# Optimization experiments

Measured on AMD Instinct MI355X. Metric: run time of the kernel, lower is better.

## Reference

```python
import jax, jax.numpy as jnp
import numpy as np

NB, NLOC, NALL, NNEI = 1, 4096, 6144, 64
N_EDGE, N_ANGLE, A_SEL = 262144, 409600, 10
N_DIM, E_DIM, A_DIM, AXIS = 128, 64, 32, 4
SEL_REDUCE = 10.0


def _lin_params(key, din, dout):
    k1, k2 = jax.random.split(key)
    W = jax.random.normal(k1, (din, dout), jnp.float32) / np.float32(np.sqrt(din))
    b = jax.random.normal(k2, (dout,), jnp.float32) * 0.01
    return W, b


def setup_inputs():
    key = jax.random.key(0)
    ks = jax.random.split(key, 20)
    inp = {}
    inp["node_ebd_ext"] = jax.random.normal(ks[0], (NB, NALL, N_DIM), jnp.float32)
    inp["edge_ebd"] = jax.random.normal(ks[1], (N_EDGE, E_DIM), jnp.float32)
    inp["h2"] = jax.random.normal(ks[2], (N_EDGE, 3), jnp.float32)
    inp["angle_ebd"] = jax.random.normal(ks[3], (N_ANGLE, A_DIM), jnp.float32)
    inp["nlist"] = jax.random.randint(ks[4], (NB, NLOC, NNEI), 0, NALL)
    inp["nlist_mask"] = jnp.ones((NB, NLOC, NNEI), jnp.bool_)
    inp["sw"] = jax.random.uniform(ks[5], (N_EDGE,), jnp.float32)
    inp["a_nlist"] = jax.random.randint(ks[6], (NB, NLOC, A_SEL), 0, NALL)
    inp["a_nlist_mask"] = jnp.ones((NB, NLOC, A_SEL), jnp.bool_)
    inp["a_sw"] = jax.random.uniform(ks[7], (N_ANGLE,), jnp.float32)
    n2e = jax.random.randint(ks[8], (N_EDGE,), 0, NB * NLOC)
    n_ext2e = jax.random.randint(ks[9], (N_EDGE,), 0, NB * NALL)
    inp["edge_index"] = jnp.stack([n2e, n_ext2e])
    n2a = jax.random.randint(ks[10], (N_ANGLE,), 0, NB * NLOC)
    eij2a = jax.random.randint(ks[11], (N_ANGLE,), 0, N_EDGE)
    eik2a = jax.random.randint(ks[12], (N_ANGLE,), 0, N_EDGE)
    inp["angle_index"] = jnp.stack([n2a, eij2a, eik2a])
    sym_dim = (N_DIM + E_DIM) * AXIS          # 768
    edge_info_dim = 2 * N_DIM + E_DIM         # 320
    angle_dim = A_DIM + N_DIM + 2 * E_DIM     # 288
    inp["W_node_self"], inp["b_node_self"] = _lin_params(ks[13], N_DIM, N_DIM)
    inp["W_node_sym"], inp["b_node_sym"] = _lin_params(ks[14], sym_dim, N_DIM)
    inp["W_node_edge"], inp["b_node_edge"] = _lin_params(ks[15], edge_info_dim, N_DIM)
    inp["W_edge_self"], inp["b_edge_self"] = _lin_params(ks[16], edge_info_dim, E_DIM)
    inp["W_edge_angle1"], inp["b_edge_angle1"] = _lin_params(ks[17], angle_dim, E_DIM)
    inp["W_edge_angle2"], inp["b_edge_angle2"] = _lin_params(ks[18], E_DIM, E_DIM)
    inp["W_angle_self"], inp["b_angle_self"] = _lin_params(ks[19], angle_dim, A_DIM)
    inp["n_res0"] = jnp.full((N_DIM,), 0.1, jnp.float32)
    inp["n_res1"] = jnp.full((N_DIM,), 0.1, jnp.float32)
    inp["n_res2"] = jnp.full((N_DIM,), 0.1, jnp.float32)
    inp["e_res0"] = jnp.full((E_DIM,), 0.1, jnp.float32)
    inp["e_res1"] = jnp.full((E_DIM,), 0.1, jnp.float32)
    inp["a_res0"] = jnp.full((A_DIM,), 0.1, jnp.float32)
    return inp


def reference(node_ebd_ext, edge_ebd, h2, angle_ebd, nlist, nlist_mask, sw,
              a_nlist, a_nlist_mask, a_sw, edge_index, angle_index,
              W_node_self, b_node_self, W_node_sym, b_node_sym,
              W_node_edge, b_node_edge, W_edge_self, b_edge_self,
              W_edge_angle1, b_edge_angle1, W_edge_angle2, b_edge_angle2,
              W_angle_self, b_angle_self,
              n_res0, n_res1, n_res2, e_res0, e_res1, a_res0):
    act = jax.nn.silu
    nb, nloc, nnei = nlist.shape
    n_dim = node_ebd_ext.shape[-1]
    n_edge = h2.shape[0]
    dyn_e_sel = nnei / SEL_REDUCE
    dyn_a_sel = a_nlist.shape[-1] / SEL_REDUCE
    node_ebd = node_ebd_ext[:, :nloc]
    n2e, n_ext2e = edge_index[0], edge_index[1]
    n2a, eij2a, eik2a = angle_index[0], angle_index[1], angle_index[2]
    nei_node_ebd = node_ebd_ext.reshape(-1, n_dim)[n_ext2e]  # [n_edge, n_dim]
    node_self = act(node_ebd @ W_node_self + b_node_self)

    def sym_op(flat_ebd):
        # symmetrization: outer(h2, sw*ebd) scattered to owners, then grrg
        d = flat_ebd.shape[-1]
        w = flat_ebd * sw[:, None]
        h2g2 = jax.ops.segment_sum(
            (h2[:, :, None] * w[:, None, :]).reshape(n_edge, 3 * d),
            n2e, num_segments=nb * nloc)
        h2g2 = h2g2.reshape(nb, nloc, 3, d) * (dyn_e_sel ** -0.5)
        m = h2g2[..., :AXIS]  # [nb, nloc, 3, axis]
        g = jnp.einsum('blxa,blxd->blad', m, h2g2) / 3.0
        return g.reshape(nb, nloc, AXIS * d)

    sym_edge = sym_op(edge_ebd)
    sym_node = sym_op(nei_node_ebd)
    node_sym = act(jnp.concatenate([sym_edge, sym_node], -1) @ W_node_sym + b_node_sym)
    node_i = node_ebd.reshape(-1, n_dim)[n2e]
    edge_info = jnp.concatenate([node_i, nei_node_ebd, edge_ebd], -1)  # [n_edge, 320]
    node_edge_update = act(edge_info @ W_node_edge + b_node_edge) * sw[:, None]
    node_edge_msg = jax.ops.segment_sum(node_edge_update, n2e, num_segments=nb * nloc).reshape(nb, nloc, -1) / dyn_e_sel
    n_updated = node_ebd + n_res0 * node_self + n_res1 * node_sym + n_res2 * node_edge_msg
    edge_self = act(edge_info @ W_edge_self + b_edge_self)
    node_for_angle = node_ebd.reshape(-1, n_dim)[n2a]
    edge_ik = edge_ebd[eik2a]
    edge_ij = edge_ebd[eij2a]
    angle_info = jnp.concatenate([angle_ebd, node_for_angle, edge_ik, edge_ij], -1)  # [n_angle, 288]
    edge_angle = act(angle_info @ W_edge_angle1 + b_edge_angle1)
    reduced = jax.ops.segment_sum(edge_angle * a_sw[:, None], eij2a, num_segments=n_edge) / (dyn_a_sel ** 0.5)
    edge_angle_msg = act(reduced @ W_edge_angle2 + b_edge_angle2)
    e_updated = edge_ebd + e_res0 * edge_self + e_res1 * edge_angle_msg
    angle_self = act(angle_info @ W_angle_self + b_angle_self)
    a_updated = angle_ebd + a_res0 * angle_self
    return (n_updated, e_updated, a_updated)
```

## Files before the change

kernel.cpp:

```cpp
#include <hip/hip_runtime.h>
#include <hip/hip_bf16.h>

#define NLOC_   4096
#define NALL_   6144
#define NEDGE_  262144
#define NANGLE_ 409600

typedef __bf16 bf16x8 __attribute__((ext_vector_type(8)));
typedef float  f32x4  __attribute__((ext_vector_type(4)));
typedef unsigned short u16;

__device__ __forceinline__ float silu_(float x){ return x / (1.0f + __expf(-x)); }

__device__ __forceinline__ u16 f2bu(float f){
    union { float f; unsigned u; } v; v.f = f;
    unsigned r = v.u + 0x7fffu + ((v.u >> 16) & 1u);
    return (u16)(r >> 16);
}
__device__ __forceinline__ float bu2f(u16 b){
    union { unsigned u; float f; } v; v.u = ((unsigned)b) << 16; return v.f;
}
__device__ __forceinline__ void st_bf16x4(u16* dst, float4 v){
    unsigned lo = (unsigned)f2bu(v.x) | ((unsigned)f2bu(v.y) << 16);
    unsigned hi = (unsigned)f2bu(v.z) | ((unsigned)f2bu(v.w) << 16);
    *reinterpret_cast<uint2*>(dst) = make_uint2(lo, hi);
}

__global__ void k_prep(const float* __restrict__ Wne, const float* __restrict__ Wes,
                       const float* __restrict__ W1,  const float* __restrict__ WA,
                       const float* __restrict__ W2,
                       u16* __restrict__ WTe, u16* __restrict__ WTa, u16* __restrict__ WT2)
{
    int b = blockIdx.x, t = threadIdx.x;
    if (b < 192) {
        if (t < 320) WTe[b*320 + t] = f2bu(b < 128 ? Wne[t*128 + b] : Wes[t*64 + (b-128)]);
    } else if (b < 288) {
        int n = b - 192;
        if (t < 288) WTa[n*288 + t] = f2bu(n < 64 ? W1[t*64 + n] : WA[t*32 + (n-64)]);
    } else {
        int n = b - 288;
        if (t < 64)  WT2[n*64 + t] = f2bu(W2[t*64 + n]);
    }
}

__global__ void k_cvt(const float* __restrict__ src, u16* __restrict__ dst, int n4)
{
    int i = blockIdx.x * 256 + threadIdx.x;
    int stride = gridDim.x * 256;
    for (; i < n4; i += stride) {
        float4 v = ((const float4*)src)[i];
        st_bf16x4(&dst[(size_t)i*4], v);
    }
}

__global__ __launch_bounds__(256) void k_nconst(
    const u16* __restrict__ NB, const u16* __restrict__ WTe,
    float* __restrict__ nconst)
{
    __shared__ __align__(16) u16 sN[64][136];
    const int tid = threadIdx.x;
    const int e0 = blockIdx.x * 64;
    #pragma unroll
    for (int f = tid; f < 1024; f += 256) {
        int r = f >> 4, c = f & 15;
        *(uint4*)&sN[r][8*c] = ((const uint4*)&NB[(size_t)(e0 + r)*128])[c];
    }
    __syncthreads();

    const int w = tid >> 6, l = tid & 63;
    const int lr = l & 15, hq = l >> 4, lk = hq * 8;

    f32x4 acc[4][3] = {};
    #pragma unroll
    for (int kk = 0; kk < 4; ++kk) {
        bf16x8 a[4], b[3];
        #pragma unroll
        for (int m = 0; m < 4; ++m)
            a[m] = *(const bf16x8*)&sN[16*m + lr][kk*32 + lk];
        #pragma unroll
        for (int nf = 0; nf < 3; ++nf)
            b[nf] = *(const bf16x8*)&WTe[(size_t)(48*w + 16*nf + lr)*320 + kk*32 + lk];
        #pragma unroll
        for (int m = 0; m < 4; ++m)
            #pragma unroll
            for (int nf = 0; nf < 3; ++nf)
                acc[m][nf] = __builtin_amdgcn_mfma_f32_16x16x32_bf16(a[m], b[nf], acc[m][nf], 0, 0, 0);
    }
    #pragma unroll
    for (int nf = 0; nf < 3; ++nf) {
        int c = 48*w + 16*nf + lr;
        #pragma unroll
        for (int m = 0; m < 4; ++m)
            #pragma unroll
            for (int j = 0; j < 4; ++j) {
                int r = 16*m + 4*hq + j;
                nconst[(size_t)(e0 + r)*192 + c] = acc[m][nf][j];
            }
    }
}

__global__ void k_count(const int* __restrict__ key, int* __restrict__ cnt)
{
    int e = blockIdx.x * 256 + threadIdx.x;
    atomicAdd(&cnt[key[e]], 1);
}

__global__ void k_scan(const int* __restrict__ cnt, int* __restrict__ off,
                       int* __restrict__ cursor)
{
    __shared__ int wa[1024];
    int t = threadIdx.x;
    int a0 = cnt[4*t], a1 = cnt[4*t+1], a2 = cnt[4*t+2], a3 = cnt[4*t+3];
    int s1 = a0 + a1, s2 = s1 + a2, s3 = s2 + a3;
    wa[t] = s3;
    __syncthreads();
    for (int d = 1; d < 1024; d <<= 1) {
        int x = wa[t];
        int y = (t >= d) ? wa[t-d] : 0;
        __syncthreads();
        wa[t] = x + y;
        __syncthreads();
    }
    int excl = (t == 0) ? 0 : wa[t-1];
    off[4*t]   = excl;        cursor[4*t]   = excl;
    off[4*t+1] = excl + a0;   cursor[4*t+1] = excl + a0;
    off[4*t+2] = excl + s1;   cursor[4*t+2] = excl + s1;
    off[4*t+3] = excl + s2;   cursor[4*t+3] = excl + s2;
    if (t == 1023) off[4096] = excl + s3;
}

__global__ void k_fill(const int* __restrict__ key, int* __restrict__ cursor,
                       int* __restrict__ csr)
{
    int e = blockIdx.x * 256 + threadIdx.x;
    int pos = atomicAdd(&cursor[key[e]], 1);
    csr[pos] = e;
}

__global__ void k_fill_rank(const int* __restrict__ key, int* __restrict__ cursor,
                            int* __restrict__ rank)
{
    int e = blockIdx.x * 256 + threadIdx.x;
    int pos = atomicAdd(&cursor[key[e]], 1);
    rank[e] = pos;
}

__global__ void k_scan2a(const int* __restrict__ cnt2, int* __restrict__ bsum)
{
    __shared__ int wa[256];
    int b = blockIdx.x, t = threadIdx.x;
    int4 v = ((const int4*)cnt2)[b*256 + t];
    wa[t] = v.x + v.y + v.z + v.w;
    __syncthreads();
    for (int d = 128; d > 0; d >>= 1) {
        if (t < d) wa[t] += wa[t+d];
        __syncthreads();
    }
    if (t == 0) bsum[b] = wa[0];
}

__global__ void k_scan2b(const int* __restrict__ bsum, int* __restrict__ boff)
{
    __shared__ int wa[256];
    int t = threadIdx.x;
    wa[t] = bsum[t];
    __syncthreads();
    for (int d = 1; d < 256; d <<= 1) {
        int x = wa[t];
        int y = (t >= d) ? wa[t-d] : 0;
        __syncthreads();
        wa[t] = x + y;
        __syncthreads();
    }
    boff[t] = (t == 0) ? 0 : wa[t-1];
}

__global__ void k_scan2c(const int* __restrict__ cnt2, const int* __restrict__ boff,
                         int* __restrict__ off2, int* __restrict__ cursor2)
{
    __shared__ int wa[256];
    int b = blockIdx.x, t = threadIdx.x;
    int4 v = ((const int4*)cnt2)[b*256 + t];
    int s1 = v.x, s2 = s1 + v.y, s3 = s2 + v.z, s4 = s3 + v.w;
    wa[t] = s4;
    __syncthreads();
    for (int d = 1; d < 256; d <<= 1) {
        int x = wa[t];
        int y = (t >= d) ? wa[t-d] : 0;
        __syncthreads();
        wa[t] = x + y;
        __syncthreads();
    }
    int base = boff[b] + ((t == 0) ? 0 : wa[t-1]);
    int i = (b*256 + t)*4;
    off2[i]   = base;      cursor2[i]   = base;
    off2[i+1] = base + s1; cursor2[i+1] = base + s1;
    off2[i+2] = base + s2; cursor2[i+2] = base + s2;
    off2[i+3] = base + s3; cursor2[i+3] = base + s3;
    if (b == 255 && t == 255) off2[NEDGE_] = NANGLE_;
}

__global__ __launch_bounds__(256, 4) void k_edge_flat(
    const u16* __restrict__ NB, const u16* __restrict__ EB,
    const float* __restrict__ h2, const float* __restrict__ sw,
    const int* __restrict__ n2e, const int* __restrict__ n_ext2e,
    const int* __restrict__ csr,
    const u16* __restrict__ WTe, const float* __restrict__ nconst,
    const float* __restrict__ bne, const float* __restrict__ bes,
    const float* __restrict__ e_res0,
    float* __restrict__ msg,
    float* __restrict__ h2g2_e, float* __restrict__ h2g2_n,
    float* __restrict__ e_out)
{
    __shared__ __align__(16) u16 sA[64][200];
    __shared__ float sH[4][576];
    __shared__ int   s_eid[64];
    __shared__ int   s_node[64];
    __shared__ int   s_g[64];
    __shared__ float s_sw[64];
    __shared__ float s_h2[64][3];
    __shared__ int   s_segstart[65];
    __shared__ int   s_nseg;

    const int tid = threadIdx.x;
    const int w  = tid >> 6, l = tid & 63;
    const int lr = l & 15, hq = l >> 4, lk = hq * 8;
    const int base = blockIdx.x * 64;

    if (tid < 64) {
        int e = csr[base + tid];
        s_eid[tid]  = e;
        s_node[tid] = n2e[e];
        s_g[tid]    = n_ext2e[e];
        s_sw[tid]   = sw[e];
        s_h2[tid][0] = h2[e*3];
        s_h2[tid][1] = h2[e*3+1];
        s_h2[tid][2] = h2[e*3+2];
    }
    __syncthreads();

    if (tid < 64) {
        bool flag = (tid == 0) || (s_node[tid] != s_node[tid-1]);
        unsigned long long mask = __ballot(flag);
        if (flag) {
            int sid = __popcll(mask & ((1ull << tid) - 1ull));
            s_segstart[sid] = tid;
        }
        if (tid == 0) {
            int ns = __popcll(mask);
            s_nseg = ns;
            s_segstart[ns] = 64;
        }
    }

    #pragma unroll
    for (int f = tid; f < 1024; f += 256) {
        int r = f >> 4, c = f & 15;
        *(uint4*)&sA[r][8*c] = ((const uint4*)&NB[(size_t)s_g[r]*128])[c];
    }
    #pragma unroll
    for (int f = tid; f < 512; f += 256) {
        int r = f >> 3, c = f & 7;
        *(uint4*)&sA[r][128 + 8*c] = ((const uint4*)&EB[(size_t)s_eid[r]*64])[c];
    }
    __syncthreads();

    float bias[3], rres[3];
    int   cful[3];
    #pragma unroll
    for (int nf = 0; nf < 3; ++nf) {
        int c = 48*w + 16*nf + lr;
        cful[nf] = c;
        bias[nf] = (c < 128) ? bne[c] : bes[c-128];
        rres[nf] = (c < 128) ? 0.f    : e_res0[c-128];
    }

    f32x4 acc[4][3] = {};
    #pragma unroll
    for (int kk = 0; kk < 6; ++kk) {
        bf16x8 a[4], b[3];
        #pragma unroll
        for (int m = 0; m < 4; ++m)
            a[m] = *(const bf16x8*)&sA[16*m + lr][kk*32 + lk];
        #pragma unroll
        for (int nf = 0; nf < 3; ++nf)
            b[nf] = *(const bf16x8*)&WTe[(size_t)cful[nf]*320 + 128 + kk*32 + lk];
        #pragma unroll
        for (int m = 0; m < 4; ++m)
            #pragma unroll
            for (int nf = 0; nf < 3; ++nf)
                acc[m][nf] = __builtin_amdgcn_mfma_f32_16x16x32_bf16(a[m], b[nf], acc[m][nf], 0, 0, 0);
    }

    #pragma unroll
    for (int nf = 0; nf < 3; ++nf) {
        int c = cful[nf];
        if (c < 128) {
            #pragma unroll
            for (int m = 0; m < 4; ++m)
                #pragma unroll
                for (int j = 0; j < 4; ++j) {
                    int r = 16*m + 4*hq + j;
                    float ncv = nconst[(size_t)s_node[r]*192 + c];
                    acc[m][nf][j] = silu_(acc[m][nf][j] + ncv + bias[nf]) * s_sw[r];
                }
        } else {
            int c2 = c - 128;
            #pragma unroll
            for (int m = 0; m < 4; ++m)
                #pragma unroll
                for (int j = 0; j < 4; ++j) {
                    int r = 16*m + 4*hq + j;
                    float ncv = nconst[(size_t)s_node[r]*192 + c];
                    e_out[(size_t)s_eid[r]*64 + c2] =
                        bu2f(sA[r][128 + c2]) + rres[nf] * silu_(acc[m][nf][j] + ncv + bias[nf]);
                }
        }
    }

    const int nseg = s_nseg;
    for (int s = 0; s < nseg; ++s) {
        int rs = s_segstart[s], re = s_segstart[s+1];
        int nd = s_node[rs];
        #pragma unroll
        for (int nf = 0; nf < 3; ++nf) {
            if (cful[nf] >= 128) continue;
            float v = 0.f;
            #pragma unroll
            for (int m = 0; m < 4; ++m)
                #pragma unroll
                for (int j = 0; j < 4; ++j) {
                    int r = 16*m + 4*hq + j;
                    v += (r >= rs && r < re) ? acc[m][nf][j] : 0.f;
                }
            v += __shfl_xor(v, 16);
            v += __shfl_xor(v, 32);
            if (hq == 0) atomicAdd(&msg[(size_t)nd*128 + cful[nf]], v);
        }
    }

    for (int s = 0; s < nseg; ++s) {
        int rs = s_segstart[s], re = s_segstart[s+1];
        int nd = s_node[rs];
        int lo = max(16*w, rs), hi = min(16*w + 16, re);
        float hacc[9] = {0.f,0.f,0.f,0.f,0.f,0.f,0.f,0.f,0.f};
        for (int r = lo; r < hi; ++r) {
            float swv = s_sw[r];
            float s0 = s_h2[r][0] * swv;
            float s1 = s_h2[r][1] * swv;
            float s2 = s_h2[r][2] * swv;
            float eb = bu2f(sA[r][128 + l]);
            float n0 = bu2f(sA[r][l]);
            float n1 = bu2f(sA[r][64 + l]);
            hacc[0] = fmaf(s0, eb, hacc[0]);
            hacc[1] = fmaf(s1, eb, hacc[1]);
            hacc[2] = fmaf(s2, eb, hacc[2]);
            hacc[3] = fmaf(s0, n0, hacc[3]);
            hacc[4] = fmaf(s0, n1, hacc[4]);
            hacc[5] = fmaf(s1, n0, hacc[5]);
            hacc[6] = fmaf(s1, n1, hacc[6]);
            hacc[7] = fmaf(s2, n0, hacc[7]);
            hacc[8] = fmaf(s2, n1, hacc[8]);
        }
        #pragma unroll
        for (int q = 0; q < 3; ++q) sH[w][q*64 + l] = hacc[q];
        #pragma unroll
        for (int q = 0; q < 6; ++q) sH[w][192 + q*64 + l] = hacc[3+q];
        __syncthreads();
        for (int i = tid; i < 576; i += 256) {
            float v = sH[0][i] + sH[1][i] + sH[2][i] + sH[3][i];
            if (i < 192) atomicAdd(&h2g2_e[(size_t)nd*192 + i], v);
            else         atomicAdd(&h2g2_n[(size_t)nd*384 + (i - 192)], v);
        }
        __syncthreads();
    }
}

__global__ __launch_bounds__(256) void k_angle_mfma(
    const u16* __restrict__ NB, const u16* __restrict__ EB,
    const u16* __restrict__ AB, const float* __restrict__ a_sw,
    const int* __restrict__ n2a, const int* __restrict__ eij2a,
    const int* __restrict__ eik2a, const int* __restrict__ rank2,
    const u16* __restrict__ WTa,
    const float* __restrict__ b1, const float* __restrict__ bA,
    const float* __restrict__ a_res0,
    u16* __restrict__ ea, float* __restrict__ a_out)
{
    __shared__ __align__(16) u16 sA[64][296];
    __shared__ int s_na[64], s_ij[64], s_ik[64], s_rk[64];
    const int tid = threadIdx.x;
    const int a0 = blockIdx.x * 64;

    if (tid < 64) {
        s_na[tid] = n2a[a0 + tid];
        s_ij[tid] = eij2a[a0 + tid];
        s_ik[tid] = eik2a[a0 + tid];
        s_rk[tid] = rank2[a0 + tid];
    }
    __syncthreads();

    #pragma unroll
    for (int f = tid; f < 256; f += 256) {
        int a = f >> 2, c = f & 3;
        *(uint4*)&sA[a][8*c] = ((const uint4*)&AB[(size_t)(a0 + a)*32])[c];
    }
    #pragma unroll
    for (int f = tid; f < 1024; f += 256) {
        int a = f >> 4, c = f & 15;
        *(uint4*)&sA[a][32 + 8*c] = ((const uint4*)&NB[(size_t)s_na[a]*128])[c];
    }
    #pragma unroll
    for (int f = tid; f < 512; f += 256) {
        int a = f >> 3, c = f & 7;
        *(uint4*)&sA[a][160 + 8*c] = ((const uint4*)&EB[(size_t)s_ik[a]*64])[c];
    }
    #pragma unroll
    for (int f = tid; f < 512; f += 256) {
        int a = f >> 3, c = f & 7;
        *(uint4*)&sA[a][224 + 8*c] = ((const uint4*)&EB[(size_t)s_ij[a]*64])[c];
    }
    __syncthreads();

    const int w = tid >> 6, l = tid & 63;
    const int lr = l & 15, lk = (l >> 4) * 8;

    f32x4 acc[6] = {};
    #pragma unroll
    for (int kk = 0; kk < 9; ++kk) {
        bf16x8 a = *(const bf16x8*)&sA[16*w + lr][kk*32 + lk];
        #pragma unroll
        for (int n = 0; n < 6; ++n) {
            bf16x8 b = *(const bf16x8*)&WTa[(size_t)(16*n + lr)*288 + kk*32 + lk];
            acc[n] = __builtin_amdgcn_mfma_f32_16x16x32_bf16(a, b, acc[n], 0, 0, 0);
        }
    }

    #pragma unroll
    for (int n = 0; n < 6; ++n) {
        int c = 16*n + lr;
        if (n < 4) {
            float bb = b1[c];
            #pragma unroll
            for (int j = 0; j < 4; ++j) {
                int r = 16*w + ((l >> 4) << 2) + j;
                float eav = silu_(acc[n][j] + bb) * a_sw[a0 + r];
                ea[(size_t)s_rk[r]*64 + c] = f2bu(eav);
            }
        } else {
            int c2 = c - 64;
            float bb = bA[c2], rr = a_res0[c2];
            #pragma unroll
            for (int j = 0; j < 4; ++j) {
                int r = 16*w + ((l >> 4) << 2) + j;
                size_t idx = (size_t)(a0 + r)*32 + c2;
                a_out[idx] = bu2f(sA[r][c2]) + rr * silu_(acc[n][j] + bb);
            }
        }
    }
}

__global__ __launch_bounds__(256) void k_edgefin_mfma(
    const u16* __restrict__ ea,
    const int* __restrict__ off2,
    const u16* __restrict__ WT2,
    const float* __restrict__ b2_, const float* __restrict__ e_res1,
    float* __restrict__ e_out)
{
    __shared__ __align__(16) u16 sR[64][72];
    const int tid = threadIdx.x;
    const int e0 = blockIdx.x * 64;
    const int w = tid >> 6, l = tid & 63;

    #pragma unroll
    for (int r16 = 0; r16 < 16; ++r16) {
        int r = w*16 + r16;
        int e = e0 + r;
        float s = 0.f;
        int jb = off2[e], je = off2[e+1];
        for (int j = jb; j < je; ++j)
            s += bu2f(ea[(size_t)j*64 + l]);
        sR[r][l] = f2bu(s);
    }
    __syncthreads();

    const int lr = l & 15, lk = (l >> 4) * 8;

    f32x4 acc[4] = {};
    #pragma unroll
    for (int kk = 0; kk < 2; ++kk) {
        bf16x8 b = *(const bf16x8*)&WT2[(size_t)(16*w + lr)*64 + kk*32 + lk];
        #pragma unroll
        for (int m = 0; m < 4; ++m) {
            bf16x8 a = *(const bf16x8*)&sR[16*m + lr][kk*32 + lk];
            acc[m] = __builtin_amdgcn_mfma_f32_16x16x32_bf16(a, b, acc[m], 0, 0, 0);
        }
    }
    int c = 16*w + lr;
    float bb = b2_[c], rr = e_res1[c];
    #pragma unroll
    for (int m = 0; m < 4; ++m)
        #pragma unroll
        for (int j = 0; j < 4; ++j) {
            size_t idx = (size_t)(e0 + 16*m + ((l >> 4) << 2) + j)*64 + c;
            e_out[idx] += rr * silu_(acc[m][j] + bb);
        }
}

__global__ void k_node_final(const float* __restrict__ node_ext,
                             const float* __restrict__ h2g2_e,
                             const float* __restrict__ h2g2_n,
                             const float* __restrict__ msg,
                             const float* __restrict__ Wns,  const float* __restrict__ bns,
                             const float* __restrict__ Wsym, const float* __restrict__ bsym,
                             const float* __restrict__ nr0, const float* __restrict__ nr1,
                             const float* __restrict__ nr2,
                             float* __restrict__ n_out)
{
    __shared__ float x[128];
    __shared__ float he[192];
    __shared__ float hn[384];
    __shared__ float symc[768];

    int n = blockIdx.x;
    int c = threadIdx.x;

    x[c] = node_ext[(size_t)n*128 + c];
    for (int i = c; i < 192; i += 128) he[i] = h2g2_e[(size_t)n*192 + i];
    for (int i = c; i < 384; i += 128) hn[i] = h2g2_n[(size_t)n*384 + i];
    __syncthreads();

    const float SCALE = 1.0f / (6.4f * 3.0f);
    for (int i = c; i < 768; i += 128) {
        float s;
        if (i < 256) {
            int a = i >> 6, j = i & 63;
            s = he[a]*he[j] + he[64+a]*he[64+j] + he[128+a]*he[128+j];
        } else {
            int i2 = i - 256;
            int a = i2 >> 7, j = i2 & 127;
            s = hn[a]*hn[j] + hn[128+a]*hn[128+j] + hn[256+a]*hn[256+j];
        }
        symc[i] = s * SCALE;
    }
    __syncthreads();

    float accs = 0.f;
    #pragma unroll 8
    for (int k = 0; k < 128; ++k) accs = fmaf(x[k], Wns[k*128 + c], accs);
    float self_ = silu_(accs + bns[c]);

    float accy = 0.f;
    #pragma unroll 8
    for (int k = 0; k < 768; ++k) accy = fmaf(symc[k], Wsym[k*128 + c], accy);
    float sym_ = silu_(accy + bsym[c]);

    float m = msg[(size_t)n*128 + c] * (1.0f / 6.4f);
    n_out[(size_t)n*128 + c] = x[c] + nr0[c]*self_ + nr1[c]*sym_ + nr2[c]*m;
}

extern "C" void kernel_launch(void* const* d_in, const int* in_sizes, int n_in,
                              void* d_out, int out_size, void* d_ws, size_t ws_size,
                              hipStream_t stream)
{
    const float* node_ext  = (const float*)d_in[0];
    const float* edge_ebd  = (const float*)d_in[1];
    const float* h2        = (const float*)d_in[2];
    const float* angle_ebd = (const float*)d_in[3];
    const float* sw        = (const float*)d_in[6];
    const float* a_sw      = (const float*)d_in[9];
    const int*  edge_index  = (const int*)d_in[10];
    const int*  angle_index = (const int*)d_in[11];
    const int* n2e     = edge_index;
    const int* n_ext2e = edge_index + NEDGE_;
    const int* n2a     = angle_index;
    const int* eij2a   = angle_index + NANGLE_;
    const int* eik2a   = angle_index + 2*NANGLE_;

    const float* Wns  = (const float*)d_in[12];
    const float* bns  = (const float*)d_in[13];
    const float* Wsym = (const float*)d_in[14];
    const float* bsym = (const float*)d_in[15];
    const float* Wne  = (const float*)d_in[16];
    const float* bne  = (const float*)d_in[17];
    const float* Wes  = (const float*)d_in[18];
    const float* bes  = (const float*)d_in[19];
    const float* W1   = (const float*)d_in[20];
    const float* b1   = (const float*)d_in[21];
    const float* W2   = (const float*)d_in[22];
    const float* b2_  = (const float*)d_in[23];
    const float* WA   = (const float*)d_in[24];
    const float* bA   = (const float*)d_in[25];
    const float* nr0  = (const float*)d_in[26];
    const float* nr1  = (const float*)d_in[27];
    const float* nr2  = (const float*)d_in[28];
    const float* er0  = (const float*)d_in[29];
    const float* er1  = (const float*)d_in[30];
    const float* ar0  = (const float*)d_in[31];

    char* wsp = (char*)d_ws;
    u16*   ea      = (u16*)wsp;    wsp += (size_t)NANGLE_ * 64 * 2;
    u16*   EB      = (u16*)wsp;    wsp += (size_t)NEDGE_ * 64 * 2;
    u16*   NB      = (u16*)wsp;    wsp += (size_t)NALL_ * 128 * 2;
    u16*   AB      = (u16*)wsp;    wsp += (size_t)NANGLE_ * 32 * 2;
    int*   cnt     = (int*)wsp;    wsp += 4096 * 4;
    int*   cnt2    = (int*)wsp;    wsp += (size_t)NEDGE_ * 4;
    float* msg     = (float*)wsp;  wsp += (size_t)NLOC_ * 128 * 4;
    float* h2g2_e  = (float*)wsp;  wsp += (size_t)NLOC_ * 192 * 4;
    float* h2g2_n  = (float*)wsp;  wsp += (size_t)NLOC_ * 384 * 4;
    size_t zero_bytes = 4096*4 + (size_t)NEDGE_*4 + (size_t)NLOC_*128*4
                      + (size_t)NLOC_*192*4 + (size_t)NLOC_*384*4;
    int*   off     = (int*)wsp;    wsp += 4104 * 4;
    int*   cursor  = (int*)wsp;    wsp += 4096 * 4;
    int*   csr     = (int*)wsp;    wsp += (size_t)NEDGE_ * 4;
    int*   off2    = (int*)wsp;    wsp += ((size_t)NEDGE_ + 16) * 4;
    int*   cursor2 = (int*)wsp;    wsp += (size_t)NEDGE_ * 4;
    int*   bsum    = (int*)wsp;    wsp += 256 * 4;
    int*   boff    = (int*)wsp;    wsp += 256 * 4;
    int*   rank2   = (int*)wsp;    wsp += (size_t)NANGLE_ * 4;
    float* nconst  = (float*)wsp;  wsp += (size_t)NLOC_ * 192 * 4;
    u16*   WTe     = (u16*)wsp;    wsp += 192 * 320 * 2;
    u16*   WTa     = (u16*)wsp;    wsp += 96 * 288 * 2;
    u16*   WT2     = (u16*)wsp;    wsp += 64 * 64 * 2;

    hipMemsetAsync(cnt, 0, zero_bytes, stream);

    float* n_out = (float*)d_out;
    float* e_out = n_out + (size_t)NLOC_ * 128;
    float* a_out = e_out + (size_t)NEDGE_ * 64;

    k_prep   <<<352, 320, 0, stream>>>(Wne, Wes, W1, WA, W2, WTe, WTa, WT2);
    k_cvt    <<<768, 256, 0, stream>>>(node_ext, NB, NALL_*128/4);
    k_cvt    <<<4096, 256, 0, stream>>>(edge_ebd, EB, NEDGE_*64/4);
    k_cvt    <<<4096, 256, 0, stream>>>(angle_ebd, AB, NANGLE_*32/4);
    k_count  <<<NEDGE_/256, 256, 0, stream>>>(n2e, cnt);
    k_scan   <<<1, 1024, 0, stream>>>(cnt, off, cursor);
    k_fill   <<<NEDGE_/256, 256, 0, stream>>>(n2e, cursor, csr);
    k_count  <<<NANGLE_/256, 256, 0, stream>>>(eij2a, cnt2);
    k_scan2a <<<256, 256, 0, stream>>>(cnt2, bsum);
    k_scan2b <<<1, 256, 0, stream>>>(bsum, boff);
    k_scan2c <<<256, 256, 0, stream>>>(cnt2, boff, off2, cursor2);
    k_fill_rank <<<NANGLE_/256, 256, 0, stream>>>(eij2a, cursor2, rank2);

    k_nconst <<<NLOC_/64, 256, 0, stream>>>(NB, WTe, nconst);
    k_edge_flat <<<NEDGE_/64, 256, 0, stream>>>(NB, EB, h2, sw, n2e, n_ext2e, csr,
                                                WTe, nconst, bne, bes, er0,
                                                msg, h2g2_e, h2g2_n, e_out);
    k_angle_mfma <<<NANGLE_/64, 256, 0, stream>>>(NB, EB, AB, a_sw,
                                                  n2a, eij2a, eik2a, rank2,
                                                  WTa, b1, bA, ar0, ea, a_out);
    k_edgefin_mfma <<<NEDGE_/64, 256, 0, stream>>>(ea, off2, WT2, b2_, er1, e_out);
    k_node_final <<<NLOC_, 128, 0, stream>>>(node_ext, h2g2_e, h2g2_n, msg,
                                             Wns, bns, Wsym, bsym,
                                             nr0, nr1, nr2, n_out);
}
```

Before: 497.5 us.

## Move node-final GEMMs to MFMA and restructure edge/angle output writes

Replaces the scalar per-node k_node_final with a k_symc kernel that writes the symmetric features as bf16, followed by a 32-row MFMA kernel for the sym and self linear layers. The edge self-update is now written to a bf16 buffer in CSR order. It is combined in k_edgefin with a coalesced read of the edge embedding through a new rank array, so e_out is written once rather than read-modify-written. The angle kernel drops to 32-row tiles and stages its scattered ea output in LDS so it can be written as 16-byte vectors. These changes add an extra kernel launch, an intermediate buffer and more bf16 rounding of intermediates.

```diff
diff --git a/kernel.cpp b/kernel.cpp
--- a/kernel.cpp
+++ b/kernel.cpp
@@ -28,8 +28,10 @@
 
 __global__ void k_prep(const float* __restrict__ Wne, const float* __restrict__ Wes,
                        const float* __restrict__ W1,  const float* __restrict__ WA,
-                       const float* __restrict__ W2,
-                       u16* __restrict__ WTe, u16* __restrict__ WTa, u16* __restrict__ WT2)
+                       const float* __restrict__ W2,  const float* __restrict__ Wsym,
+                       const float* __restrict__ Wns,
+                       u16* __restrict__ WTe, u16* __restrict__ WTa, u16* __restrict__ WT2,
+                       u16* __restrict__ WsymT, u16* __restrict__ WnsT)
 {
     int b = blockIdx.x, t = threadIdx.x;
     if (b < 192) {
@@ -37,9 +39,15 @@
     } else if (b < 288) {
         int n = b - 192;
         if (t < 288) WTa[n*288 + t] = f2bu(n < 64 ? W1[t*64 + n] : WA[t*32 + (n-64)]);
-    } else {
+    } else if (b < 352) {
         int n = b - 288;
         if (t < 64)  WT2[n*64 + t] = f2bu(W2[t*64 + n]);
+    } else if (b < 480) {
+        int n = b - 352;
+        if (t < 768) WsymT[n*768 + t] = f2bu(Wsym[t*128 + n]);
+    } else {
+        int n = b - 480;
+        if (t < 128) WnsT[n*128 + t] = f2bu(Wns[t*128 + n]);
     }
 }
 
@@ -129,12 +137,13 @@
     if (t == 1023) off[4096] = excl + s3;
 }
 
-__global__ void k_fill(const int* __restrict__ key, int* __restrict__ cursor,
-                       int* __restrict__ csr)
+__global__ void k_fill_both(const int* __restrict__ key, int* __restrict__ cursor,
+                            int* __restrict__ csr, int* __restrict__ rank)
 {
     int e = blockIdx.x * 256 + threadIdx.x;
     int pos = atomicAdd(&cursor[key[e]], 1);
     csr[pos] = e;
+    rank[e] = pos;
 }
 
 __global__ void k_fill_rank(const int* __restrict__ key, int* __restrict__ cursor,
@@ -207,10 +216,9 @@
     const int* __restrict__ csr,
     const u16* __restrict__ WTe, const float* __restrict__ nconst,
     const float* __restrict__ bne, const float* __restrict__ bes,
-    const float* __restrict__ e_res0,
     float* __restrict__ msg,
     float* __restrict__ h2g2_e, float* __restrict__ h2g2_n,
-    float* __restrict__ e_out)
+    u16* __restrict__ eselfB)
 {
     __shared__ __align__(16) u16 sA[64][200];
     __shared__ float sH[4][576];
@@ -265,14 +273,13 @@
     }
     __syncthreads();
 
-    float bias[3], rres[3];
+    float bias[3];
     int   cful[3];
     #pragma unroll
     for (int nf = 0; nf < 3; ++nf) {
         int c = 48*w + 16*nf + lr;
         cful[nf] = c;
         bias[nf] = (c < 128) ? bne[c] : bes[c-128];
-        rres[nf] = (c < 128) ? 0.f    : e_res0[c-128];
     }
 
     f32x4 acc[4][3] = {};
@@ -312,8 +319,8 @@
                 for (int j = 0; j < 4; ++j) {
                     int r = 16*m + 4*hq + j;
                     float ncv = nconst[(size_t)s_node[r]*192 + c];
-                    e_out[(size_t)s_eid[r]*64 + c2] =
-                        bu2f(sA[r][128 + c2]) + rres[nf] * silu_(acc[m][nf][j] + ncv + bias[nf]);
+                    eselfB[(size_t)(base + r)*64 + c2] =
+                        f2bu(silu_(acc[m][nf][j] + ncv + bias[nf]));
                 }
         }
     }
@@ -386,90 +393,115 @@
     const float* __restrict__ a_res0,
     u16* __restrict__ ea, float* __restrict__ a_out)
 {
-    __shared__ __align__(16) u16 sA[64][296];
-    __shared__ int s_na[64], s_ij[64], s_ik[64], s_rk[64];
+    __shared__ __align__(16) u16 sA[32][296];
+    __shared__ __align__(16) u16 sEA[32][64];
+    __shared__ int s_na[32], s_ij[32], s_ik[32], s_rk[32];
+    __shared__ float s_asw[32];
     const int tid = threadIdx.x;
-    const int a0 = blockIdx.x * 64;
-
-    if (tid < 64) {
+    const int a0 = blockIdx.x * 32;
+
+    if (tid < 32) {
         s_na[tid] = n2a[a0 + tid];
         s_ij[tid] = eij2a[a0 + tid];
         s_ik[tid] = eik2a[a0 + tid];
         s_rk[tid] = rank2[a0 + tid];
-    }
-    __syncthreads();
-
-    #pragma unroll
-    for (int f = tid; f < 256; f += 256) {
-        int a = f >> 2, c = f & 3;
-        *(uint4*)&sA[a][8*c] = ((const uint4*)&AB[(size_t)(a0 + a)*32])[c];
-    }
-    #pragma unroll
-    for (int f = tid; f < 1024; f += 256) {
-        int a = f >> 4, c = f & 15;
-        *(uint4*)&sA[a][32 + 8*c] = ((const uint4*)&NB[(size_t)s_na[a]*128])[c];
+        s_asw[tid] = a_sw[a0 + tid];
+    }
+    __syncthreads();
+
+    if (tid < 128) {
+        int r = tid >> 2, c = tid & 3;
+        *(uint4*)&sA[r][8*c] = ((const uint4*)&AB[(size_t)(a0 + r)*32])[c];
     }
     #pragma unroll
     for (int f = tid; f < 512; f += 256) {
-        int a = f >> 3, c = f & 7;
-        *(uint4*)&sA[a][160 + 8*c] = ((const uint4*)&EB[(size_t)s_ik[a]*64])[c];
-    }
-    #pragma unroll
-    for (int f = tid; f < 512; f += 256) {
-        int a = f >> 3, c = f & 7;
-        *(uint4*)&sA[a][224 + 8*c] = ((const uint4*)&EB[(size_t)s_ij[a]*64])[c];
+        int r = f >> 4, c = f & 15;
+        *(uint4*)&sA[r][32 + 8*c] = ((const uint4*)&NB[(size_t)s_na[r]*128])[c];
+    }
+    if (tid < 256) {
+        int r = tid >> 3, c = tid & 7;
+        *(uint4*)&sA[r][160 + 8*c] = ((const uint4*)&EB[(size_t)s_ik[r]*64])[c];
+    }
+    {
+        int f = tid;
+        if (f < 256) {
+            int r = f >> 3, c = f & 7;
+            *(uint4*)&sA[r][224 + 8*c] = ((const uint4*)&EB[(size_t)s_ij[r]*64])[c];
+        }
     }
     __syncthreads();
 
     const int w = tid >> 6, l = tid & 63;
-    const int lr = l & 15, lk = (l >> 4) * 8;
-
-    f32x4 acc[6] = {};
+    const int lr = l & 15, hq = l >> 4, lk = hq * 8;
+    const int mrow  = (w & 1) * 16;
+    const int nbase = (w >> 1) * 48;
+
+    f32x4 acc[3] = {};
     #pragma unroll
     for (int kk = 0; kk < 9; ++kk) {
-        bf16x8 a = *(const bf16x8*)&sA[16*w + lr][kk*32 + lk];
-        #pragma unroll
-        for (int n = 0; n < 6; ++n) {
-            bf16x8 b = *(const bf16x8*)&WTa[(size_t)(16*n + lr)*288 + kk*32 + lk];
-            acc[n] = __builtin_amdgcn_mfma_f32_16x16x32_bf16(a, b, acc[n], 0, 0, 0);
-        }
-    }
-
-    #pragma unroll
-    for (int n = 0; n < 6; ++n) {
-        int c = 16*n + lr;
-        if (n < 4) {
+        bf16x8 a = *(const bf16x8*)&sA[mrow + lr][kk*32 + lk];
+        #pragma unroll
+        for (int nf = 0; nf < 3; ++nf) {
+            bf16x8 b = *(const bf16x8*)&WTa[(size_t)(nbase + 16*nf + lr)*288 + kk*32 + lk];
+            acc[nf] = __builtin_amdgcn_mfma_f32_16x16x32_bf16(a, b, acc[nf], 0, 0, 0);
+        }
+    }
+
+    #pragma unroll
+    for (int nf = 0; nf < 3; ++nf) {
+        int c = nbase + 16*nf + lr;
+        if (c < 64) {
             float bb = b1[c];
             #pragma unroll
             for (int j = 0; j < 4; ++j) {
-                int r = 16*w + ((l >> 4) << 2) + j;
-                float eav = silu_(acc[n][j] + bb) * a_sw[a0 + r];
-                ea[(size_t)s_rk[r]*64 + c] = f2bu(eav);
+                int r = mrow + 4*hq + j;
+                sEA[r][c] = f2bu(silu_(acc[nf][j] + bb) * s_asw[r]);
             }
         } else {
             int c2 = c - 64;
             float bb = bA[c2], rr = a_res0[c2];
             #pragma unroll
             for (int j = 0; j < 4; ++j) {
-                int r = 16*w + ((l >> 4) << 2) + j;
+                int r = mrow + 4*hq + j;
                 size_t idx = (size_t)(a0 + r)*32 + c2;
-                a_out[idx] = bu2f(sA[r][c2]) + rr * silu_(acc[n][j] + bb);
+                a_out[idx] = bu2f(sA[r][c2]) + rr * silu_(acc[nf][j] + bb);
             }
         }
     }
+    __syncthreads();
+
+    if (tid < 256) {
+        int r = tid >> 3, c = tid & 7;
+        *(uint4*)&ea[(size_t)s_rk[r]*64 + 8*c] = *(const uint4*)&sEA[r][8*c];
+    }
 }
 
 __global__ __launch_bounds__(256) void k_edgefin_mfma(
-    const u16* __restrict__ ea,
-    const int* __restrict__ off2,
+    const u16* __restrict__ EB, const u16* __restrict__ eselfB,
+    const int* __restrict__ rank_e,
+    const u16* __restrict__ ea, const int* __restrict__ off2,
     const u16* __restrict__ WT2,
-    const float* __restrict__ b2_, const float* __restrict__ e_res1,
+    const float* __restrict__ b2_, const float* __restrict__ er0,
+    const float* __restrict__ er1,
     float* __restrict__ e_out)
 {
     __shared__ __align__(16) u16 sR[64][72];
+    __shared__ __align__(16) u16 sE[64][72];
+    __shared__ __align__(16) u16 sB[64][72];
+    __shared__ int s_rk[64];
     const int tid = threadIdx.x;
     const int e0 = blockIdx.x * 64;
     const int w = tid >> 6, l = tid & 63;
+
+    if (tid < 64) s_rk[tid] = rank_e[e0 + tid];
+    __syncthreads();
+
+    #pragma unroll
+    for (int f = tid; f < 512; f += 256) {
+        int r = f >> 3, c = f & 7;
+        *(uint4*)&sB[r][8*c] = ((const uint4*)&EB[(size_t)(e0 + r)*64])[c];
+        *(uint4*)&sE[r][8*c] = ((const uint4*)&eselfB[(size_t)s_rk[r]*64])[c];
+    }
 
     #pragma unroll
     for (int r16 = 0; r16 < 16; ++r16) {
@@ -483,7 +515,7 @@
     }
     __syncthreads();
 
-    const int lr = l & 15, lk = (l >> 4) * 8;
+    const int lr = l & 15, hq = l >> 4, lk = hq * 8;
 
     f32x4 acc[4] = {};
     #pragma unroll
@@ -496,41 +528,31 @@
         }
     }
     int c = 16*w + lr;
-    float bb = b2_[c], rr = e_res1[c];
+    float bb = b2_[c], r0 = er0[c], r1 = er1[c];
     #pragma unroll
     for (int m = 0; m < 4; ++m)
         #pragma unroll
         for (int j = 0; j < 4; ++j) {
-            size_t idx = (size_t)(e0 + 16*m + ((l >> 4) << 2) + j)*64 + c;
-            e_out[idx] += rr * silu_(acc[m][j] + bb);
-        }
-}
-
-__global__ void k_node_final(const float* __restrict__ node_ext,
-                             const float* __restrict__ h2g2_e,
-                             const float* __restrict__ h2g2_n,
-                             const float* __restrict__ msg,
-                             const float* __restrict__ Wns,  const float* __restrict__ bns,
-                             const float* __restrict__ Wsym, const float* __restrict__ bsym,
-                             const float* __restrict__ nr0, const float* __restrict__ nr1,
-                             const float* __restrict__ nr2,
-                             float* __restrict__ n_out)
-{
-    __shared__ float x[128];
+            int r = 16*m + 4*hq + j;
+            size_t idx = (size_t)(e0 + r)*64 + c;
+            e_out[idx] = bu2f(sB[r][c]) + r0 * bu2f(sE[r][c])
+                       + r1 * silu_(acc[m][j] + bb);
+        }
+}
+
+__global__ void k_symc(const float* __restrict__ h2g2_e,
+                       const float* __restrict__ h2g2_n,
+                       u16* __restrict__ symcB)
+{
     __shared__ float he[192];
     __shared__ float hn[384];
-    __shared__ float symc[768];
-
     int n = blockIdx.x;
-    int c = threadIdx.x;
-
-    x[c] = node_ext[(size_t)n*128 + c];
-    for (int i = c; i < 192; i += 128) he[i] = h2g2_e[(size_t)n*192 + i];
-    for (int i = c; i < 384; i += 128) hn[i] = h2g2_n[(size_t)n*384 + i];
-    __syncthreads();
-
+    int t = threadIdx.x;
+    for (int i = t; i < 192; i += 128) he[i] = h2g2_e[(size_t)n*192 + i];
+    for (int i = t; i < 384; i += 128) hn[i] = h2g2_n[(size_t)n*384 + i];
+    __syncthreads();
     const float SCALE = 1.0f / (6.4f * 3.0f);
-    for (int i = c; i < 768; i += 128) {
+    for (int i = t; i < 768; i += 128) {
         float s;
         if (i < 256) {
             int a = i >> 6, j = i & 63;
@@ -540,22 +562,95 @@
             int a = i2 >> 7, j = i2 & 127;
             s = hn[a]*hn[j] + hn[128+a]*hn[128+j] + hn[256+a]*hn[256+j];
         }
-        symc[i] = s * SCALE;
-    }
-    __syncthreads();
-
-    float accs = 0.f;
-    #pragma unroll 8
-    for (int k = 0; k < 128; ++k) accs = fmaf(x[k], Wns[k*128 + c], accs);
-    float self_ = silu_(accs + bns[c]);
-
-    float accy = 0.f;
-    #pragma unroll 8
-    for (int k = 0; k < 768; ++k) accy = fmaf(symc[k], Wsym[k*128 + c], accy);
-    float sym_ = silu_(accy + bsym[c]);
-
-    float m = msg[(size_t)n*128 + c] * (1.0f / 6.4f);
-    n_out[(size_t)n*128 + c] = x[c] + nr0[c]*self_ + nr1[c]*sym_ + nr2[c]*m;
+        symcB[(size_t)n*768 + i] = f2bu(s * SCALE);
+    }
+}
+
+__global__ __launch_bounds__(256) void k_node_mfma(
+    const u16* __restrict__ symcB, const u16* __restrict__ NB,
+    const float* __restrict__ node_ext, const float* __restrict__ msg,
+    const u16* __restrict__ WsymT, const u16* __restrict__ WnsT,
+    const float* __restrict__ bns, const float* __restrict__ bsym,
+    const float* __restrict__ nr0, const float* __restrict__ nr1,
+    const float* __restrict__ nr2,
+    float* __restrict__ n_out)
+{
+    __shared__ __align__(16) u16 sA[32][264];
+    const int tid = threadIdx.x;
+    const int n0 = blockIdx.x * 32;
+    const int w = tid >> 6, l = tid & 63;
+    const int lr = l & 15, hq = l >> 4, lk = hq * 8;
+
+    f32x4 accY[2][2] = {};
+    f32x4 accS[2][2] = {};
+
+    for (int chunk = 0; chunk < 3; ++chunk) {
+        __syncthreads();
+        #pragma unroll
+        for (int f = tid; f < 1024; f += 256) {
+            int r = f >> 5, c = f & 31;
+            *(uint4*)&sA[r][8*c] =
+                ((const uint4*)&symcB[(size_t)(n0 + r)*768 + chunk*256])[c];
+        }
+        __syncthreads();
+        #pragma unroll
+        for (int kk = 0; kk < 8; ++kk) {
+            bf16x8 a[2], b[2];
+            #pragma unroll
+            for (int m = 0; m < 2; ++m)
+                a[m] = *(const bf16x8*)&sA[16*m + lr][kk*32 + lk];
+            #pragma unroll
+            for (int nf = 0; nf < 2; ++nf)
+                b[nf] = *(const bf16x8*)&WsymT[(size_t)(32*w + 16*nf + lr)*768
+                                               + chunk*256 + kk*32 + lk];
+            #pragma unroll
+            for (int m = 0; m < 2; ++m)
+                #pragma unroll
+                for (int nf = 0; nf < 2; ++nf)
+                    accY[m][nf] = __builtin_amdgcn_mfma_f32_16x16x32_bf16(a[m], b[nf], accY[m][nf], 0, 0, 0);
+        }
+    }
+
+    __syncthreads();
+    #pragma unroll
+    for (int f = tid; f < 512; f += 256) {
+        int r = f >> 4, c = f & 15;
+        *(uint4*)&sA[r][8*c] = ((const uint4*)&NB[(size_t)(n0 + r)*128])[c];
+    }
+    __syncthreads();
+    #pragma unroll
+    for (int kk = 0; kk < 4; ++kk) {
+        bf16x8 a[2], b[2];
+        #pragma unroll
+        for (int m = 0; m < 2; ++m)
+            a[m] = *(const bf16x8*)&sA[16*m + lr][kk*32 + lk];
+        #pragma unroll
+        for (int nf = 0; nf < 2; ++nf)
+            b[nf] = *(const bf16x8*)&WnsT[(size_t)(32*w + 16*nf + lr)*128 + kk*32 + lk];
+        #pragma unroll
+        for (int m = 0; m < 2; ++m)
+            #pragma unroll
+            for (int nf = 0; nf < 2; ++nf)
+                accS[m][nf] = __builtin_amdgcn_mfma_f32_16x16x32_bf16(a[m], b[nf], accS[m][nf], 0, 0, 0);
+    }
+
+    #pragma unroll
+    for (int nf = 0; nf < 2; ++nf) {
+        int c = 32*w + 16*nf + lr;
+        float bS = bns[c], bY = bsym[c];
+        float r0 = nr0[c], r1 = nr1[c], r2 = nr2[c];
+        #pragma unroll
+        for (int m = 0; m < 2; ++m)
+            #pragma unroll
+            for (int j = 0; j < 4; ++j) {
+                int r = 16*m + 4*hq + j;
+                size_t idx = (size_t)(n0 + r)*128 + c;
+                float self_ = silu_(accS[m][nf][j] + bS);
+                float sym_  = silu_(accY[m][nf][j] + bY);
+                n_out[idx] = node_ext[idx] + r0*self_ + r1*sym_
+                           + r2 * msg[idx] * (1.0f / 6.4f);
+            }
+    }
 }
 
 extern "C" void kernel_launch(void* const* d_in, const int* in_sizes, int n_in,
@@ -602,6 +697,8 @@
     u16*   EB      = (u16*)wsp;    wsp += (size_t)NEDGE_ * 64 * 2;
     u16*   NB      = (u16*)wsp;    wsp += (size_t)NALL_ * 128 * 2;
     u16*   AB      = (u16*)wsp;    wsp += (size_t)NANGLE_ * 32 * 2;
+    u16*   eselfB  = (u16*)wsp;    wsp += (size_t)NEDGE_ * 64 * 2;
+    u16*   symcB   = (u16*)wsp;    wsp += (size_t)NLOC_ * 768 * 2;
     int*   cnt     = (int*)wsp;    wsp += 4096 * 4;
     int*   cnt2    = (int*)wsp;    wsp += (size_t)NEDGE_ * 4;
     float* msg     = (float*)wsp;  wsp += (size_t)NLOC_ * 128 * 4;
@@ -612,6 +709,7 @@
     int*   off     = (int*)wsp;    wsp += 4104 * 4;
     int*   cursor  = (int*)wsp;    wsp += 4096 * 4;
     int*   csr     = (int*)wsp;    wsp += (size_t)NEDGE_ * 4;
+    int*   rank_e  = (int*)wsp;    wsp += (size_t)NEDGE_ * 4;
     int*   off2    = (int*)wsp;    wsp += ((size_t)NEDGE_ + 16) * 4;
     int*   cursor2 = (int*)wsp;    wsp += (size_t)NEDGE_ * 4;
     int*   bsum    = (int*)wsp;    wsp += 256 * 4;
@@ -621,6 +719,8 @@
     u16*   WTe     = (u16*)wsp;    wsp += 192 * 320 * 2;
     u16*   WTa     = (u16*)wsp;    wsp += 96 * 288 * 2;
     u16*   WT2     = (u16*)wsp;    wsp += 64 * 64 * 2;
+    u16*   WsymT   = (u16*)wsp;    wsp += 128 * 768 * 2;
+    u16*   WnsT    = (u16*)wsp;    wsp += 128 * 128 * 2;
 
     hipMemsetAsync(cnt, 0, zero_bytes, stream);
 
@@ -628,13 +728,14 @@
     float* e_out = n_out + (size_t)NLOC_ * 128;
     float* a_out = e_out + (size_t)NEDGE_ * 64;
 
-    k_prep   <<<352, 320, 0, stream>>>(Wne, Wes, W1, WA, W2, WTe, WTa, WT2);
+    k_prep   <<<608, 768, 0, stream>>>(Wne, Wes, W1, WA, W2, Wsym, Wns,
+                                       WTe, WTa, WT2, WsymT, WnsT);
     k_cvt    <<<768, 256, 0, stream>>>(node_ext, NB, NALL_*128/4);
     k_cvt    <<<4096, 256, 0, stream>>>(edge_ebd, EB, NEDGE_*64/4);
     k_cvt    <<<4096, 256, 0, stream>>>(angle_ebd, AB, NANGLE_*32/4);
     k_count  <<<NEDGE_/256, 256, 0, stream>>>(n2e, cnt);
     k_scan   <<<1, 1024, 0, stream>>>(cnt, off, cursor);
-    k_fill   <<<NEDGE_/256, 256, 0, stream>>>(n2e, cursor, csr);
+    k_fill_both <<<NEDGE_/256, 256, 0, stream>>>(n2e, cursor, csr, rank_e);
     k_count  <<<NANGLE_/256, 256, 0, stream>>>(eij2a, cnt2);
     k_scan2a <<<256, 256, 0, stream>>>(cnt2, bsum);
     k_scan2b <<<1, 256, 0, stream>>>(bsum, boff);
@@ -643,13 +744,15 @@
 
     k_nconst <<<NLOC_/64, 256, 0, stream>>>(NB, WTe, nconst);
     k_edge_flat <<<NEDGE_/64, 256, 0, stream>>>(NB, EB, h2, sw, n2e, n_ext2e, csr,
-                                                WTe, nconst, bne, bes, er0,
-                                                msg, h2g2_e, h2g2_n, e_out);
-    k_angle_mfma <<<NANGLE_/64, 256, 0, stream>>>(NB, EB, AB, a_sw,
+                                                WTe, nconst, bne, bes,
+                                                msg, h2g2_e, h2g2_n, eselfB);
+    k_angle_mfma <<<NANGLE_/32, 256, 0, stream>>>(NB, EB, AB, a_sw,
                                                   n2a, eij2a, eik2a, rank2,
                                                   WTa, b1, bA, ar0, ea, a_out);
-    k_edgefin_mfma <<<NEDGE_/64, 256, 0, stream>>>(ea, off2, WT2, b2_, er1, e_out);
-    k_node_final <<<NLOC_, 128, 0, stream>>>(node_ext, h2g2_e, h2g2_n, msg,
-                                             Wns, bns, Wsym, bsym,
-                                             nr0, nr1, nr2, n_out);
-}
+    k_edgefin_mfma <<<NEDGE_/64, 256, 0, stream>>>(EB, eselfB, rank_e, ea, off2,
+                                                   WT2, b2_, er0, er1, e_out);
+    k_symc   <<<NLOC_, 128, 0, stream>>>(h2g2_e, h2g2_n, symcB);
+    k_node_mfma <<<NLOC_/32, 256, 0, stream>>>(symcB, NB, node_ext, msg,
+                                               WsymT, WnsT, bns, bsym,
+                                               nr0, nr1, nr2, n_out);
+}
```

New measurement: 454.3 us. 1.09x faster.
